# Performance work log

Measured on AMD Instinct MI355X. Metric: run time of the kernel, lower is better.

## Reference

```python
import jax, jax.numpy as jnp
import numpy as np

N = 50000
E = 1600000
IN_F = 512
OUT_F = 128
NEG_SLOPE = 0.01   # nn.LeakyReLU() default
TEMPERATURE = 0.5


def setup_inputs() -> dict:
    key = jax.random.key(0)
    k1, k2, k3, k4 = jax.random.split(key, 4)
    h = jax.random.normal(k1, (N, IN_F), dtype=jnp.float32)
    # xavier_uniform with gain=1.414
    limW = 1.414 * np.sqrt(6.0 / (IN_F + OUT_F))
    W = jax.random.uniform(k2, (IN_F, OUT_F), minval=-limW, maxval=limW, dtype=jnp.float32)
    lima = 1.414 * np.sqrt(6.0 / (2 * OUT_F + 1))
    a = jax.random.uniform(k3, (2 * OUT_F, 1), minval=-lima, maxval=lima, dtype=jnp.float32)
    edge_index = jax.random.randint(k4, (2, E), 0, N, dtype=jnp.int64)
    return {"h": h, "W": W, "a": a, "edge_index": edge_index}


def reference(h, W, a, edge_index):
    # Inference: F.dropout(training=False) is identity.
    Wh = h @ W                                   # [N, F_out]
    src = edge_index[0]                          # row indices -> softmax segments
    dst = edge_index[1]
    # cat([Wh[src], Wh[dst]]) @ a == (Wh @ a1)[src] + (Wh @ a2)[dst]
    a1 = a[:OUT_F, 0]
    a2 = a[OUT_F:, 0]
    s1 = Wh @ a1                                 # [N]
    s2 = Wh @ a2                                 # [N]
    e = s1[src] + s2[dst]                        # [E]
    e = jnp.where(e >= 0, e, NEG_SLOPE * e)      # LeakyReLU
    logits = e / TEMPERATURE
    # sparse softmax over dim=1 (per source-node row segments)
    seg_max = jax.ops.segment_max(logits, src, num_segments=N)  # [N]
    ex = jnp.exp(logits - seg_max[src])          # [E]
    denom = jax.ops.segment_sum(ex, src, num_segments=N)        # [N]
    att = ex / denom[src]                        # [E]
    # sparse-dense matmul: h_prime[i] = sum_j att(i,j) * Wh[j]
    h_prime = jax.ops.segment_sum(att[:, None] * Wh[dst], src, num_segments=N)  # [N, F_out]
    return jax.nn.relu(h_prime)                  # concat=True path
```

## Files before the change

kernel.cpp:

```cpp
#include <hip/hip_runtime.h>
#include <cstdint>
#include <cstddef>

#define N_NODES 50000
#define N_EDGES 1600000
#define IN_FEAT 512
#define OUT_FEAT 128
#define NEG_SLOPE 0.01f
#define INV_TEMP 2.0f
#define PAD_DEG 128

#define BUCKETS 400
#define BNODES 125
#define BCAP 5000
#define A_BLOCKS 500
#define A_EPC (N_EDGES / A_BLOCKS)
#define A_G4 (A_EPC / 4)

#define CONV_BLOCKS ((IN_FEAT * OUT_FEAT) / 256)
#define GEMM_BLOCKS ((N_NODES + 63) / 64)

typedef __attribute__((ext_vector_type(8))) short short8;
typedef __attribute__((ext_vector_type(4))) float f32x4;

#define GLOBAL_AS __attribute__((address_space(1)))
#define LDS_AS __attribute__((address_space(3)))

__device__ inline unsigned short f2bf(float x) {
    unsigned int u = __float_as_uint(x);
    unsigned int r = (u + 0x7fffu + ((u >> 16) & 1u)) >> 16;
    return (unsigned short)r;
}
__device__ inline float bf2f(unsigned short b) {
    return __uint_as_float(((unsigned int)b) << 16);
}


__global__ __launch_bounds__(256) void build_kernel(const float* __restrict__ W,
                                                    unsigned short* __restrict__ Wt,
                                                    const int* __restrict__ src,
                                                    const int* __restrict__ dst,
                                                    int* __restrict__ bucket_cursor,
                                                    int* __restrict__ binned) {
    __shared__ int cntL[BUCKETS];
    __shared__ int baseL[BUCKETS];

    if (blockIdx.x >= A_BLOCKS) {
        int tid = (blockIdx.x - A_BLOCKS) * 256 + threadIdx.x;
        if (tid < IN_FEAT * OUT_FEAT) {
            int n = tid >> 9;
            int k = tid & 511;
            Wt[tid] = f2bf(W[k * OUT_FEAT + n]);
        }
        return;
    }

    int t = threadIdx.x;
    for (int i = t; i < BUCKETS; i += 256) cntL[i] = 0;
    __syncthreads();
    size_t ebase = (size_t)blockIdx.x * A_EPC;

    for (int g = t; g < A_G4; g += 256) {
        int4 s4 = *(const int4*)(src + ebase + (size_t)g * 4);
#pragma unroll
        for (int j = 0; j < 4; ++j) {
            int s = (&s4.x)[j];
            atomicAdd(&cntL[s / BNODES], 1);
        }
    }
    __syncthreads();
    for (int i = t; i < BUCKETS; i += 256) {
        int c = cntL[i];
        baseL[i] = c ? atomicAdd(&bucket_cursor[i], c) : 0;
        cntL[i] = 0;
    }
    __syncthreads();
    for (int g = t; g < A_G4; g += 256) {
        int4 s4 = *(const int4*)(src + ebase + (size_t)g * 4);
        int4 d4 = *(const int4*)(dst + ebase + (size_t)g * 4);
#pragma unroll
        for (int j = 0; j < 4; ++j) {
            int s = (&s4.x)[j];
            int b = s / BNODES;
            int sl = s - b * BNODES;
            int pos = atomicAdd(&cntL[b], 1);
            int slot = baseL[b] + pos;
            if (slot < BCAP)
                binned[(size_t)b * BCAP + slot] = (sl << 16) | (&d4.x)[j];
        }
    }
}


__global__ __launch_bounds__(256) void gemm_binB_kernel(const float* __restrict__ h,
                                                        const unsigned short* __restrict__ Wt,
                                                        const float* __restrict__ a_vec,
                                                        unsigned short* __restrict__ Whb,
                                                        float* __restrict__ s1,
                                                        float* __restrict__ s2,
                                                        const int* __restrict__ bucket_cursor,
                                                        const int* __restrict__ binned,
                                                        int* __restrict__ cnt,
                                                        int* __restrict__ csr) {
    __shared__ unsigned short lB[2][8 * 2 * 64 * 8];

    if (blockIdx.x < BUCKETS) {
        int* cL = (int*)&lB[0][0];
        int b = blockIdx.x;
        int t = threadIdx.x;
        if (t < BNODES) cL[t] = 0;
        __syncthreads();
        int m = min(bucket_cursor[b], BCAP);
        const int* bp = binned + (size_t)b * BCAP;
        int n0 = b * BNODES;
        for (int i = t; i < m; i += 256) {
            int p = bp[i];
            int sl = p >> 16;
            int d = p & 0xFFFF;
            int pos = atomicAdd(&cL[sl], 1);
            if (pos < PAD_DEG) csr[(size_t)(n0 + sl) * PAD_DEG + pos] = d;
        }
        __syncthreads();
        if (t < BNODES) cnt[n0 + t] = min(cL[t], PAD_DEG);
        return;
    }

    int bid = blockIdx.x - BUCKETS;
    int t = threadIdx.x;
    int w = t >> 6;
    int L = t & 63;
    int m0 = bid * 64;

    int arow = m0 + w * 16 + (L & 15);
    bool arow_ok = arow < N_NODES;
    int kq = (L >> 4) * 8;
    const float* arp = h + (size_t)arow * IN_FEAT + kq;

    f32x4 acc[8];
#pragma unroll
    for (int i = 0; i < 8; ++i) acc[i] = (f32x4){0.f, 0.f, 0.f, 0.f};

    auto stageB = [&](int buf, int k0) {
#pragma unroll
        for (int c = 0; c < 4; ++c) {
            int nb = w * 2 + (c >> 1);
            int ksub = c & 1;
            const GLOBAL_AS unsigned short* g =
                (const GLOBAL_AS unsigned short*)(Wt + (size_t)(nb * 16 + (L & 15)) * IN_FEAT +
                                                  (k0 + ksub * 32 + kq));
            LDS_AS unsigned short* lp = (LDS_AS unsigned short*)(&lB[buf][(nb * 2 + ksub) * 512]);
            __builtin_amdgcn_global_load_lds((const GLOBAL_AS void*)g, (LDS_AS void*)lp, 16, 0, 0);
        }
    };

    float4 av[2][2];
#pragma unroll
    for (int c = 0; c < 2; ++c) {
        av[c][0] = make_float4(0.f, 0.f, 0.f, 0.f);
        av[c][1] = make_float4(0.f, 0.f, 0.f, 0.f);
    }
    if (arow_ok) {
        av[0][0] = *(const float4*)(arp);
        av[0][1] = *(const float4*)(arp + 4);
        av[1][0] = *(const float4*)(arp + 32);
        av[1][1] = *(const float4*)(arp + 36);
    }
    stageB(0, 0);
    __syncthreads();

#pragma unroll
    for (int it = 0; it < 8; ++it) {
        const int buf = it & 1;

        if (it < 7) stageB(buf ^ 1, (it + 1) * 64);

        float4 avn[2][2];
#pragma unroll
        for (int c = 0; c < 2; ++c) {
            avn[c][0] = make_float4(0.f, 0.f, 0.f, 0.f);
            avn[c][1] = make_float4(0.f, 0.f, 0.f, 0.f);
        }
        if (it < 7 && arow_ok) {
            const float* p = arp + (it + 1) * 64;
            avn[0][0] = *(const float4*)(p);
            avn[0][1] = *(const float4*)(p + 4);
            avn[1][0] = *(const float4*)(p + 32);
            avn[1][1] = *(const float4*)(p + 36);
        }

        short8 af[2];
#pragma unroll
        for (int c = 0; c < 2; ++c) {
            short8 v;
            v[0] = (short)f2bf(av[c][0].x); v[1] = (short)f2bf(av[c][0].y);
            v[2] = (short)f2bf(av[c][0].z); v[3] = (short)f2bf(av[c][0].w);
            v[4] = (short)f2bf(av[c][1].x); v[5] = (short)f2bf(av[c][1].y);
            v[6] = (short)f2bf(av[c][1].z); v[7] = (short)f2bf(av[c][1].w);
            af[c] = v;
        }

#pragma unroll
        for (int ksub = 0; ksub < 2; ++ksub) {
#pragma unroll
            for (int nb = 0; nb < 8; ++nb) {
                short8 bf = *(const short8*)(&lB[buf][((nb * 2 + ksub) * 64 + L) * 8]);
                acc[nb] = __builtin_amdgcn_mfma_f32_16x16x32_bf16(af[ksub], bf, acc[nb], 0, 0, 0);
            }
        }

        __syncthreads();
#pragma unroll
        for (int c = 0; c < 2; ++c) {
            av[c][0] = avn[c][0];
            av[c][1] = avn[c][1];
        }
    }

    int col0 = L & 15;
    int rbase = m0 + w * 16 + (L >> 4) * 4;

    float a1c[8], a2c[8];
#pragma unroll
    for (int nb = 0; nb < 8; ++nb) {
        a1c[nb] = a_vec[nb * 16 + col0];
        a2c[nb] = a_vec[128 + nb * 16 + col0];
    }

#pragma unroll
    for (int r = 0; r < 4; ++r) {
        int row = rbase + r;
        bool ok = row < N_NODES;
        float p1 = 0.f, p2 = 0.f;
        if (ok) {
            unsigned short* orow = Whb + (size_t)row * OUT_FEAT;
#pragma unroll
            for (int nb = 0; nb < 8; ++nb) {
                float v = acc[nb][r];
                orow[nb * 16 + col0] = f2bf(v);
                p1 = fmaf(v, a1c[nb], p1);
                p2 = fmaf(v, a2c[nb], p2);
            }
        }
#pragma unroll
        for (int off = 8; off > 0; off >>= 1) {
            p1 += __shfl_xor(p1, off, 64);
            p2 += __shfl_xor(p2, off, 64);
        }
        if (ok && col0 == 0) {
            s1[row] = p1;
            s2[row] = p2;
        }
    }
}


__global__ __launch_bounds__(256) void node_kernel(const unsigned short* __restrict__ Whb,
                                                   const float* __restrict__ s1,
                                                   const float* __restrict__ s2,
                                                   const int* __restrict__ cnt,
                                                   const int* __restrict__ csr,
                                                   float* __restrict__ out) {
    int lane = threadIdx.x & 63;
    int w = threadIdx.x >> 6;
    int n = blockIdx.x * 4 + w;
    if (n >= N_NODES) return;
    int deg = cnt[n];
    size_t start = (size_t)n * PAD_DEG;
    int g = lane >> 4;
    int fo = lane & 15;

    float accv[8];
#pragma unroll
    for (int f = 0; f < 8; ++f) accv[f] = 0.f;
    float inv = 0.f;

    if (deg > 0) {
        float s1n = s1[n];
        int d0 = 0, d1 = 0;
        float ex0 = 0.f, ex1 = 0.f;
        if (lane < deg) {
            d0 = csr[start + lane];
            float ev = s1n + s2[d0];
            ev = ev >= 0.f ? ev : NEG_SLOPE * ev;
            ex0 = __expf(ev * INV_TEMP);
        }
        if (lane + 64 < deg) {
            d1 = csr[start + lane + 64];
            float ev = s1n + s2[d1];
            ev = ev >= 0.f ? ev : NEG_SLOPE * ev;
            ex1 = __expf(ev * INV_TEMP);
        }
        float denom = ex0 + ex1;
#pragma unroll
        for (int off = 32; off > 0; off >>= 1) denom += __shfl_xor(denom, off, 64);
        inv = 1.0f / denom;

#pragma unroll 2
        for (int jj = 0; jj < deg; jj += 8) {
            int e0 = jj + g;
            int e1 = jj + 4 + g;
            bool hi0 = jj >= 64;
            bool hi1 = (jj + 4) >= 64;
            float p0 = __shfl(hi0 ? ex1 : ex0, e0 & 63, 64);
            int dd0 = __shfl(hi0 ? d1 : d0, e0 & 63, 64);
            float p1 = __shfl(hi1 ? ex1 : ex0, e1 & 63, 64);
            int dd1 = __shfl(hi1 ? d1 : d0, e1 & 63, 64);
            short8 row0 = *(const short8*)(Whb + (size_t)dd0 * OUT_FEAT + fo * 8);
            short8 row1 = *(const short8*)(Whb + (size_t)dd1 * OUT_FEAT + fo * 8);
#pragma unroll
            for (int f = 0; f < 8; ++f)
                accv[f] = fmaf(p0, bf2f((unsigned short)row0[f]), accv[f]);
#pragma unroll
            for (int f = 0; f < 8; ++f)
                accv[f] = fmaf(p1, bf2f((unsigned short)row1[f]), accv[f]);
        }
#pragma unroll
        for (int f = 0; f < 8; ++f) {
            accv[f] += __shfl_xor(accv[f], 16, 64);
            accv[f] += __shfl_xor(accv[f], 32, 64);
        }
    }

    if (g == 0) {
        float* orow = out + (size_t)n * OUT_FEAT + fo * 8;
        float4 o0, o1;
        o0.x = fmaxf(accv[0] * inv, 0.f); o0.y = fmaxf(accv[1] * inv, 0.f);
        o0.z = fmaxf(accv[2] * inv, 0.f); o0.w = fmaxf(accv[3] * inv, 0.f);
        o1.x = fmaxf(accv[4] * inv, 0.f); o1.y = fmaxf(accv[5] * inv, 0.f);
        o1.z = fmaxf(accv[6] * inv, 0.f); o1.w = fmaxf(accv[7] * inv, 0.f);
        *(float4*)(orow) = o0;
        *(float4*)(orow + 4) = o1;
    }
}


extern "C" void kernel_launch(void* const* d_in, const int* in_sizes, int n_in,
                              void* d_out, int out_size, void* d_ws, size_t ws_size,
                              hipStream_t stream) {
    const float* h = (const float*)d_in[0];
    const float* W = (const float*)d_in[1];
    const float* a = (const float*)d_in[2];
    const int* edge = (const int*)d_in[3];
    const int* src = edge;
    const int* dst = edge + N_EDGES;
    float* out = (float*)d_out;

    char* ws = (char*)d_ws;
    size_t off = 0;
    auto alloc = [&](size_t bytes) -> void* {
        void* p = ws + off;
        off = (off + bytes + 255) & ~(size_t)255;
        return p;
    };
    unsigned short* Whb = (unsigned short*)alloc((size_t)N_NODES * OUT_FEAT * sizeof(unsigned short));
    float* s1 = (float*)alloc((size_t)N_NODES * sizeof(float));
    float* s2 = (float*)alloc((size_t)N_NODES * sizeof(float));
    int* cnt = (int*)alloc((size_t)N_NODES * sizeof(int));
    int* csr = (int*)alloc((size_t)N_NODES * PAD_DEG * sizeof(int));
    unsigned short* Wt = (unsigned short*)alloc((size_t)IN_FEAT * OUT_FEAT * sizeof(unsigned short));
    int* bucket_cursor = (int*)alloc((size_t)BUCKETS * sizeof(int));
    int* binned = (int*)alloc((size_t)BUCKETS * BCAP * sizeof(int));

    hipMemsetAsync(bucket_cursor, 0, BUCKETS * sizeof(int), stream);
    build_kernel<<<A_BLOCKS + CONV_BLOCKS, 256, 0, stream>>>(W, Wt, src, dst, bucket_cursor, binned);
    gemm_binB_kernel<<<BUCKETS + GEMM_BLOCKS, 256, 0, stream>>>(h, Wt, a, Whb, s1, s2,
                                                                bucket_cursor, binned, cnt, csr);
    node_kernel<<<(N_NODES + 3) / 4, 256, 0, stream>>>(Whb, s1, s2, cnt, csr, out);
}
```

Baseline: 266.6 us.

## Triple-buffer GEMM B tiles and prefetch A two steps ahead with explicit vmcnt waits

Replaces the double-buffered LDS staging of W tiles with a three-slot ring and prefetches h rows two k-steps ahead. Barriers now use hand-placed s_waitcnt vmcnt counts instead of a full __syncthreads, so later loads can stay in flight across iterations. Out-of-range rows are clamped to the last valid row instead of being masked, which removes the branch. It raises LDS use and register pressure, and correctness now depends on the hard-coded vmcnt values matching the number of loads the compiler emits.

```diff
diff --git a/kernel.cpp b/kernel.cpp
--- a/kernel.cpp
+++ b/kernel.cpp
@@ -102,7 +102,7 @@
                                                         const int* __restrict__ binned,
                                                         int* __restrict__ cnt,
                                                         int* __restrict__ csr) {
-    __shared__ unsigned short lB[2][8 * 2 * 64 * 8];
+    __shared__ unsigned short lB[3][8 * 2 * 64 * 8];
 
     if (blockIdx.x < BUCKETS) {
         int* cL = (int*)&lB[0][0];
@@ -132,15 +132,15 @@
     int m0 = bid * 64;
 
     int arow = m0 + w * 16 + (L & 15);
-    bool arow_ok = arow < N_NODES;
+    int arow_c = arow < N_NODES ? arow : N_NODES - 1;
     int kq = (L >> 4) * 8;
-    const float* arp = h + (size_t)arow * IN_FEAT + kq;
+    const float* arp = h + (size_t)arow_c * IN_FEAT + kq;
 
     f32x4 acc[8];
 #pragma unroll
     for (int i = 0; i < 8; ++i) acc[i] = (f32x4){0.f, 0.f, 0.f, 0.f};
 
-    auto stageB = [&](int buf, int k0) {
+    auto stageB = [&](int slot, int k0) {
 #pragma unroll
         for (int c = 0; c < 4; ++c) {
             int nb = w * 2 + (c >> 1);
@@ -148,71 +148,74 @@
             const GLOBAL_AS unsigned short* g =
                 (const GLOBAL_AS unsigned short*)(Wt + (size_t)(nb * 16 + (L & 15)) * IN_FEAT +
                                                   (k0 + ksub * 32 + kq));
-            LDS_AS unsigned short* lp = (LDS_AS unsigned short*)(&lB[buf][(nb * 2 + ksub) * 512]);
+            LDS_AS unsigned short* lp = (LDS_AS unsigned short*)(&lB[slot][(nb * 2 + ksub) * 512]);
             __builtin_amdgcn_global_load_lds((const GLOBAL_AS void*)g, (LDS_AS void*)lp, 16, 0, 0);
         }
     };
-
-    float4 av[2][2];
-#pragma unroll
-    for (int c = 0; c < 2; ++c) {
-        av[c][0] = make_float4(0.f, 0.f, 0.f, 0.f);
-        av[c][1] = make_float4(0.f, 0.f, 0.f, 0.f);
-    }
-    if (arow_ok) {
-        av[0][0] = *(const float4*)(arp);
-        av[0][1] = *(const float4*)(arp + 4);
-        av[1][0] = *(const float4*)(arp + 32);
-        av[1][1] = *(const float4*)(arp + 36);
-    }
+    auto loadA = [&](int step, float4 out[4]) {
+        const float* p = arp + step * 64;
+        out[0] = *(const float4*)(p);
+        out[1] = *(const float4*)(p + 4);
+        out[2] = *(const float4*)(p + 32);
+        out[3] = *(const float4*)(p + 36);
+    };
+    auto convA = [&](const float4 a[4], short8& f0, short8& f1) {
+        short8 v;
+        v[0] = (short)f2bf(a[0].x); v[1] = (short)f2bf(a[0].y);
+        v[2] = (short)f2bf(a[0].z); v[3] = (short)f2bf(a[0].w);
+        v[4] = (short)f2bf(a[1].x); v[5] = (short)f2bf(a[1].y);
+        v[6] = (short)f2bf(a[1].z); v[7] = (short)f2bf(a[1].w);
+        f0 = v;
+        v[0] = (short)f2bf(a[2].x); v[1] = (short)f2bf(a[2].y);
+        v[2] = (short)f2bf(a[2].z); v[3] = (short)f2bf(a[2].w);
+        v[4] = (short)f2bf(a[3].x); v[5] = (short)f2bf(a[3].y);
+        v[6] = (short)f2bf(a[3].z); v[7] = (short)f2bf(a[3].w);
+        f1 = v;
+    };
+
+    float4 avA[4], avB[4], avC[4];
+#pragma unroll
+    for (int q = 0; q < 4; ++q) avC[q] = make_float4(0.f, 0.f, 0.f, 0.f);
+
     stageB(0, 0);
-    __syncthreads();
+    asm volatile("" ::: "memory");
+    stageB(1, 64);
+    loadA(0, avA);
+    loadA(1, avB);
+    asm volatile("s_waitcnt vmcnt(12)" ::: "memory");
+    __builtin_amdgcn_s_barrier();
 
 #pragma unroll
     for (int it = 0; it < 8; ++it) {
-        const int buf = it & 1;
-
-        if (it < 7) stageB(buf ^ 1, (it + 1) * 64);
-
-        float4 avn[2][2];
-#pragma unroll
-        for (int c = 0; c < 2; ++c) {
-            avn[c][0] = make_float4(0.f, 0.f, 0.f, 0.f);
-            avn[c][1] = make_float4(0.f, 0.f, 0.f, 0.f);
-        }
-        if (it < 7 && arow_ok) {
-            const float* p = arp + (it + 1) * 64;
-            avn[0][0] = *(const float4*)(p);
-            avn[0][1] = *(const float4*)(p + 4);
-            avn[1][0] = *(const float4*)(p + 32);
-            avn[1][1] = *(const float4*)(p + 36);
-        }
-
-        short8 af[2];
-#pragma unroll
-        for (int c = 0; c < 2; ++c) {
-            short8 v;
-            v[0] = (short)f2bf(av[c][0].x); v[1] = (short)f2bf(av[c][0].y);
-            v[2] = (short)f2bf(av[c][0].z); v[3] = (short)f2bf(av[c][0].w);
-            v[4] = (short)f2bf(av[c][1].x); v[5] = (short)f2bf(av[c][1].y);
-            v[6] = (short)f2bf(av[c][1].z); v[7] = (short)f2bf(av[c][1].w);
-            af[c] = v;
-        }
-
-#pragma unroll
-        for (int ksub = 0; ksub < 2; ++ksub) {
-#pragma unroll
-            for (int nb = 0; nb < 8; ++nb) {
-                short8 bf = *(const short8*)(&lB[buf][((nb * 2 + ksub) * 64 + L) * 8]);
-                acc[nb] = __builtin_amdgcn_mfma_f32_16x16x32_bf16(af[ksub], bf, acc[nb], 0, 0, 0);
-            }
-        }
-
-        __syncthreads();
-#pragma unroll
-        for (int c = 0; c < 2; ++c) {
-            av[c][0] = avn[c][0];
-            av[c][1] = avn[c][1];
+        if (it < 6) {
+            stageB((it + 2) % 3, (it + 2) * 64);
+            loadA(it + 2, avC);
+        }
+
+        short8 af0, af1;
+        convA(avA, af0, af1);
+
+        const int buf = it % 3;
+#pragma unroll
+        for (int nb = 0; nb < 8; ++nb) {
+            short8 bf = *(const short8*)(&lB[buf][((nb * 2 + 0) * 64 + L) * 8]);
+            acc[nb] = __builtin_amdgcn_mfma_f32_16x16x32_bf16(af0, bf, acc[nb], 0, 0, 0);
+        }
+#pragma unroll
+        for (int nb = 0; nb < 8; ++nb) {
+            short8 bf = *(const short8*)(&lB[buf][((nb * 2 + 1) * 64 + L) * 8]);
+            acc[nb] = __builtin_amdgcn_mfma_f32_16x16x32_bf16(af1, bf, acc[nb], 0, 0, 0);
+        }
+
+#pragma unroll
+        for (int q = 0; q < 4; ++q) { avA[q] = avB[q]; avB[q] = avC[q]; }
+
+        if (it < 6) {
+            asm volatile("s_waitcnt vmcnt(8)" ::: "memory");
+            __builtin_amdgcn_s_barrier();
+        } else if (it == 6) {
+            asm volatile("s_waitcnt vmcnt(0)" ::: "memory");
+            __builtin_amdgcn_s_barrier();
         }
     }
 
```

Measured after the change: 266.1 us. About the same (-0.2%).
